# Optimization experiments

Measured on AMD Instinct MI355X. Metric: run time of the kernel, lower is better.

Reference implementation:

```python
import jax, jax.numpy as jnp
import numpy as np


def _hilbert_d2xy(n, d):
    # standard Hilbert curve: distance d -> (x, y) on n x n grid (n power of 2)
    x = y = 0
    t = d
    s = 1
    while s < n:
        rx = 1 & (t // 2)
        ry = 1 & (t ^ rx)
        if ry == 0:
            if rx == 1:
                x = s - 1 - x
                y = s - 1 - y
            x, y = y, x
        x += s * rx
        y += s * ry
        t //= 4
        s *= 2
    return x, y


def _hilbert_perm(seq_len):
    n = int(round(np.sqrt(seq_len)))
    assert n * n == seq_len
    perm = np.empty(seq_len, dtype=np.int32)
    for d in range(seq_len):
        x, y = _hilbert_d2xy(n, d)
        perm[d] = y * n + x  # linear (row-major) index visited at Hilbert step d
    return perm


def setup_inputs() -> dict:
    key = jax.random.key(0)
    k1, k2, k3 = jax.random.split(key, 3)
    B, S, H, D = 1, 4096, 8, 64
    q = jax.random.normal(k1, (B, S, H, D), dtype=jnp.float32)
    k = jax.random.normal(k2, (B, S, H, D), dtype=jnp.float32)
    v = jax.random.normal(k3, (B, S, H, D), dtype=jnp.float32)
    hilbert_perm = jnp.asarray(_hilbert_perm(S))
    return {"q": q, "k": k, "v": v, "hilbert_perm": hilbert_perm}


def reference(q, k, v, hilbert_perm):
    B, S, H, D = q.shape
    inv_perm = jnp.argsort(hilbert_perm)

    # apply_hilbert_ordering along dim=1 (seq): gather by permutation
    q_o = q[:, hilbert_perm]
    k_o = k[:, hilbert_perm]
    v_o = v[:, hilbert_perm]

    # faithful to original: raw flat reshape of [B,S,H,D] -> [B*H, S, D]
    q_f = q_o.reshape(B * H, S, D)
    k_f = k_o.reshape(B * H, S, D)
    v_f = v_o.reshape(B * H, S, D)

    scale = 1.0 / jnp.sqrt(jnp.asarray(D, dtype=q.dtype))
    scores = jnp.einsum('bsd,btd->bst', q_f, k_f) * scale  # [B*H, S, S]
    attn = jax.nn.softmax(scores, axis=-1)
    out_f = jnp.einsum('bst,btd->bsd', attn, v_f)  # [B*H, S, D]

    out = out_f.reshape(B, H, S, D).transpose(0, 2, 1, 3).reshape(B, S, H, D)
    # inverse Hilbert ordering along dim=1
    return out[:, inv_perm]
```

## Files before the change

### kernel.cpp

```cpp
#include <hip/hip_runtime.h>

typedef _Float16 f16;
typedef _Float16 f16x4 __attribute__((ext_vector_type(4)));
typedef _Float16 f16x8 __attribute__((ext_vector_type(8)));
typedef __fp16 fp16x2 __attribute__((ext_vector_type(2)));
typedef float f32x4 __attribute__((ext_vector_type(4)));

#define MFMA_16x16x32_F16(A, B, C) __builtin_amdgcn_mfma_f32_16x16x32_f16((A), (B), (C), 0, 0, 0)

typedef const __attribute__((address_space(1))) char gchar;
typedef __attribute__((address_space(3))) char lchar;

__device__ __forceinline__ float fexp2(float x) { return __builtin_amdgcn_exp2f(x); }
__device__ __forceinline__ int swzb(int b) { return b ^ ((b >> 3) & 0x70); }

namespace {
constexpr int SB = 4096;
constexpr size_t BB = (size_t)SB * 64 * 2;
}

__device__ __forceinline__ int kinv(int r) {
    return 32 * (r >> 5) + 8 * ((r >> 2) & 3) + 4 * ((r >> 4) & 1) + (r & 3);
}

__global__ __launch_bounds__(256)
void hilbert_prepass_kernel(const float* __restrict__ kp, const float* __restrict__ vp,
                            const int* __restrict__ perm,
                            char* __restrict__ kw, char* __restrict__ vtw)
{
    const int bid = blockIdx.x;
    const int batch = bid & 7;
    const int tile = bid >> 3;
    const int tid = (int)threadIdx.x;
    const int r = tid >> 2;
    const int c4 = tid & 3;

    __shared__ float Vl[64][68];

    const int t = tile * 64 + r;
    const int srow = perm[batch * 512 + (t >> 3)];
    const size_t boff = (size_t)srow * 512 + (t & 7) * 64 + c4 * 16;

    {
        const float* ks = kp + boff;
        const float4 k0 = *(const float4*)(ks + 0);
        const float4 k1 = *(const float4*)(ks + 4);
        const float4 k2 = *(const float4*)(ks + 8);
        const float4 k3 = *(const float4*)(ks + 12);
        f16x8 h0, h1;
        h0[0] = (f16)k0.x; h0[1] = (f16)k0.y; h0[2] = (f16)k0.z; h0[3] = (f16)k0.w;
        h0[4] = (f16)k1.x; h0[5] = (f16)k1.y; h0[6] = (f16)k1.z; h0[7] = (f16)k1.w;
        h1[0] = (f16)k2.x; h1[1] = (f16)k2.y; h1[2] = (f16)k2.z; h1[3] = (f16)k2.w;
        h1[4] = (f16)k3.x; h1[5] = (f16)k3.y; h1[6] = (f16)k3.z; h1[7] = (f16)k3.w;
        char* kt = kw + (size_t)batch * BB + (size_t)tile * 8192;
        const int o = r * 128 + c4 * 32;
        *(f16x8*)(kt + swzb(o)) = h0;
        *(f16x8*)(kt + swzb(o + 16)) = h1;
    }
    {
        const float* vs = vp + boff;
        *(float4*)&Vl[r][c4 * 16 + 0]  = *(const float4*)(vs + 0);
        *(float4*)&Vl[r][c4 * 16 + 4]  = *(const float4*)(vs + 4);
        *(float4*)&Vl[r][c4 * 16 + 8]  = *(const float4*)(vs + 8);
        *(float4*)&Vl[r][c4 * 16 + 12] = *(const float4*)(vs + 12);
    }
    __syncthreads();
    {
        const int d = tid >> 2;
        const int a = tid & 3;
        char* vt = vtw + (size_t)batch * BB + (size_t)tile * 8192;
        const int b0 = 32 * (a >> 1) + 4 * (a & 1);
#pragma unroll
        for (int gp = 0; gp < 4; ++gp) {
            f16x4 qv;
#pragma unroll
            for (int v = 0; v < 4; ++v) qv[v] = (f16)Vl[16 * a + 4 * gp + v][d];
            *(f16x4*)(vt + swzb(d * 128 + (b0 + 8 * gp) * 2)) = qv;
        }
    }
}

__global__ __launch_bounds__(1024, 4)
void hilbert_attn_kernel(const float* __restrict__ qp,
                         const int* __restrict__ perm,
                         const char* __restrict__ kw, const char* __restrict__ vtw,
                         float* __restrict__ op)
{
    __shared__ __align__(16) char SM[131072];

    const int bid = blockIdx.x;
    const int batch = bid & 7;
    const int qbase = (bid >> 3) * 128;
    const int tid = (int)threadIdx.x;
    const int w = tid >> 6;
    const int lane = tid & 63;
    const int l16 = lane & 15;
    const int g = lane >> 4;
    const int q = w >> 2;
    const int wq = w & 3;
    const int swz = (l16 & 7) << 4;

    f16x8 Qf0[2], Qf1[2];
    {
        constexpr float qscl = 0.125f * 1.44269504088896340736f;
#pragma unroll
        for (int s = 0; s < 2; ++s) {
            const int t = qbase + wq * 32 + s * 16 + l16;
            const int srow = perm[batch * 512 + (t >> 3)];
            const float* src = qp + (size_t)srow * 512 + (t & 7) * 64 + g * 8;
#pragma unroll
            for (int kt = 0; kt < 2; ++kt) {
                const float4 x0 = *(const float4*)(src + 32 * kt);
                const float4 x1 = *(const float4*)(src + 32 * kt + 4);
                f16x8 f;
                f[0] = (f16)(x0.x * qscl); f[1] = (f16)(x0.y * qscl);
                f[2] = (f16)(x0.z * qscl); f[3] = (f16)(x0.w * qscl);
                f[4] = (f16)(x1.x * qscl); f[5] = (f16)(x1.y * qscl);
                f[6] = (f16)(x1.z * qscl); f[7] = (f16)(x1.w * qscl);
                if (s == 0) Qf0[kt] = f; else Qf1[kt] = f;
            }
        }
    }

    f32x4 oacc0[4], oacc1[4];
#pragma unroll
    for (int i = 0; i < 4; ++i) {
        oacc0[i] = (f32x4){0.f, 0.f, 0.f, 0.f};
        oacc1[i] = (f32x4){0.f, 0.f, 0.f, 0.f};
    }
    float lr0 = 0.f, lr1 = 0.f;

    const char* ksrc = kw + (size_t)batch * BB + (size_t)tid * 16;
    const char* vsrc = vtw + (size_t)batch * BB + (size_t)tid * 16;

    {
        lchar* dst = (lchar*)&SM[w << 10];
#pragma unroll
        for (int c = 0; c < 2; ++c) {
            __builtin_amdgcn_global_load_lds((gchar*)(ksrc + c * 16384), dst + c * 16384, 16, 0, 0);
            __builtin_amdgcn_global_load_lds((gchar*)(vsrc + c * 16384), dst + 32768 + c * 16384, 16, 0, 0);
        }
    }
    __syncthreads();

#pragma unroll 2
    for (int it = 0; it < 16; ++it) {
        const int cur = it & 1;
        const int kbb = cur * 65536 + q * 8192;
        const int vbb = cur * 65536 + 32768 + q * 8192;

        if (it < 15) {
            const size_t go = (size_t)(it + 1) * 32768;
            lchar* dst = (lchar*)&SM[(cur ^ 1) * 65536 + (w << 10)];
#pragma unroll
            for (int c = 0; c < 2; ++c) {
                __builtin_amdgcn_global_load_lds((gchar*)(ksrc + go + c * 16384), dst + c * 16384, 16, 0, 0);
                __builtin_amdgcn_global_load_lds((gchar*)(vsrc + go + c * 16384), dst + 32768 + c * 16384, 16, 0, 0);
            }
        }

        f32x4 sa0[4], sa1[4];
#pragma unroll
        for (int i = 0; i < 4; ++i) {
            sa0[i] = (f32x4){0.f, 0.f, 0.f, 0.f};
            sa1[i] = (f32x4){0.f, 0.f, 0.f, 0.f};
        }
        __builtin_amdgcn_s_setprio(1);
#pragma unroll
        for (int kt = 0; kt < 2; ++kt) {
#pragma unroll
            for (int mt = 0; mt < 4; ++mt) {
                const int off = kbb + (l16 + 16 * mt) * 128 + (((g + 4 * kt) * 16) ^ swz);
                const f16x8 kf = *(const f16x8*)&SM[off];
                sa0[mt] = MFMA_16x16x32_F16(kf, Qf0[kt], sa0[mt]);
                sa1[mt] = MFMA_16x16x32_F16(kf, Qf1[kt], sa1[mt]);
            }
        }
        __builtin_amdgcn_s_setprio(0);

        float e0[16], e1[16];
#pragma unroll
        for (int mt = 0; mt < 4; ++mt) {
#pragma unroll
            for (int v = 0; v < 4; ++v) {
                e0[4 * mt + v] = fexp2(sa0[mt][v]);
                e1[4 * mt + v] = fexp2(sa1[mt][v]);
            }
        }
#pragma unroll
        for (int i = 0; i < 16; ++i) { lr0 += e0[i]; lr1 += e1[i]; }

        union U8 { f16x8 v; fp16x2 h[4]; };
        U8 p0k0, p0k1, p1k0, p1k1;
#pragma unroll
        for (int i = 0; i < 4; ++i) {
            p0k0.h[i] = __builtin_amdgcn_cvt_pkrtz(e0[2 * i], e0[2 * i + 1]);
            p0k1.h[i] = __builtin_amdgcn_cvt_pkrtz(e0[8 + 2 * i], e0[9 + 2 * i]);
            p1k0.h[i] = __builtin_amdgcn_cvt_pkrtz(e1[2 * i], e1[2 * i + 1]);
            p1k1.h[i] = __builtin_amdgcn_cvt_pkrtz(e1[8 + 2 * i], e1[9 + 2 * i]);
        }

        __builtin_amdgcn_s_setprio(1);
#pragma unroll
        for (int kt = 0; kt < 2; ++kt) {
            const f16x8 pf0 = kt ? p0k1.v : p0k0.v;
            const f16x8 pf1 = kt ? p1k1.v : p1k0.v;
#pragma unroll
            for (int mtd = 0; mtd < 4; ++mtd) {
                const int voff = vbb + (l16 + 16 * mtd) * 128 + (((g + 4 * kt) * 16) ^ swz);
                const f16x8 vf = *(const f16x8*)&SM[voff];
                oacc0[mtd] = MFMA_16x16x32_F16(vf, pf0, oacc0[mtd]);
                oacc1[mtd] = MFMA_16x16x32_F16(vf, pf1, oacc1[mtd]);
            }
        }
        __builtin_amdgcn_s_setprio(0);

        __syncthreads();
    }

    lr0 += __shfl_xor(lr0, 16);
    lr0 += __shfl_xor(lr0, 32);
    lr1 += __shfl_xor(lr1, 16);
    lr1 += __shfl_xor(lr1, 32);

    float* OB = (float*)SM;
    float* ML = (float*)&SM[98304];
    if (q >= 1) {
        float* ob = OB + ((q - 1) * 4 + wq) * 2048;
#pragma unroll
        for (int mtd = 0; mtd < 4; ++mtd) {
            *(f32x4*)&ob[l16 * 64 + mtd * 16 + g * 4] = oacc0[mtd];
            *(f32x4*)&ob[(16 + l16) * 64 + mtd * 16 + g * 4] = oacc1[mtd];
        }
        if (g == 0) {
            ML[((q - 1) * 4 + wq) * 32 + l16] = lr0;
            ML[((q - 1) * 4 + wq) * 32 + 16 + l16] = lr1;
        }
    }
    __syncthreads();
    if (q == 0) {
#pragma unroll
        for (int s = 0; s < 2; ++s) {
            float lsum = (s == 0) ? lr0 : lr1;
#pragma unroll
            for (int p = 0; p < 3; ++p) lsum += ML[(p * 4 + wq) * 32 + s * 16 + l16];
            const float linv = 1.f / lsum;
            const int t = qbase + wq * 32 + s * 16 + l16;
            const int srow = perm[t];
            float* dst = op + (size_t)srow * 512 + batch * 64 + 4 * g;
#pragma unroll
            for (int mtd = 0; mtd < 4; ++mtd) {
                f32x4 acc = (s == 0) ? oacc0[mtd] : oacc1[mtd];
#pragma unroll
                for (int p = 0; p < 3; ++p) {
                    const f32x4 o2 = *(const f32x4*)&OB[(p * 4 + wq) * 2048 +
                                                        (s * 16 + l16) * 64 + mtd * 16 + g * 4];
                    acc[0] += o2[0]; acc[1] += o2[1]; acc[2] += o2[2]; acc[3] += o2[3];
                }
                float4 o;
                o.x = acc[0] * linv; o.y = acc[1] * linv;
                o.z = acc[2] * linv; o.w = acc[3] * linv;
                *(float4*)(dst + 16 * mtd) = o;
            }
        }
    }
}

extern "C" void kernel_launch(void* const* d_in, const int* in_sizes, int n_in,
                              void* d_out, int out_size, void* d_ws, size_t ws_size,
                              hipStream_t stream) {
    (void)in_sizes; (void)n_in; (void)out_size; (void)ws_size;
    const float* q = (const float*)d_in[0];
    const float* k = (const float*)d_in[1];
    const float* v = (const float*)d_in[2];
    const int* perm = (const int*)d_in[3];
    float* out = (float*)d_out;
    char* kw = (char*)d_ws;
    char* vtw = kw + 8 * BB;
    hipLaunchKernelGGL(hilbert_prepass_kernel, dim3(512), dim3(256), 0, stream,
                       k, v, perm, kw, vtw);
    hipLaunchKernelGGL(hilbert_attn_kernel, dim3(256), dim3(1024), 0, stream,
                       q, perm, kw, vtw, out);
}
```

Baseline: 52.63 us.

## Split K and V prefetch and use fine-grained vmcnt waits with raw barriers

```diff
diff --git a/kernel.cpp b/kernel.cpp
--- a/kernel.cpp
+++ b/kernel.cpp
@@ -135,28 +135,25 @@
 
     {
         lchar* dst = (lchar*)&SM[w << 10];
-#pragma unroll
-        for (int c = 0; c < 2; ++c) {
-            __builtin_amdgcn_global_load_lds((gchar*)(ksrc + c * 16384), dst + c * 16384, 16, 0, 0);
-            __builtin_amdgcn_global_load_lds((gchar*)(vsrc + c * 16384), dst + 32768 + c * 16384, 16, 0, 0);
-        }
-    }
-    __syncthreads();
+        __builtin_amdgcn_global_load_lds((gchar*)(ksrc), dst, 16, 0, 0);
+        __builtin_amdgcn_global_load_lds((gchar*)(ksrc + 16384), dst + 16384, 16, 0, 0);
+        __builtin_amdgcn_global_load_lds((gchar*)(vsrc), dst + 32768, 16, 0, 0);
+        __builtin_amdgcn_global_load_lds((gchar*)(vsrc + 16384), dst + 49152, 16, 0, 0);
+    }
+    asm volatile("s_waitcnt vmcnt(0)" ::: "memory");
+    __builtin_amdgcn_s_barrier();
 
 #pragma unroll 2
     for (int it = 0; it < 16; ++it) {
         const int cur = it & 1;
         const int kbb = cur * 65536 + q * 8192;
         const int vbb = cur * 65536 + 32768 + q * 8192;
+        const size_t go = (size_t)(it + 1) * 32768;
+        lchar* dstb = (lchar*)&SM[(cur ^ 1) * 65536 + (w << 10)];
 
         if (it < 15) {
-            const size_t go = (size_t)(it + 1) * 32768;
-            lchar* dst = (lchar*)&SM[(cur ^ 1) * 65536 + (w << 10)];
-#pragma unroll
-            for (int c = 0; c < 2; ++c) {
-                __builtin_amdgcn_global_load_lds((gchar*)(ksrc + go + c * 16384), dst + c * 16384, 16, 0, 0);
-                __builtin_amdgcn_global_load_lds((gchar*)(vsrc + go + c * 16384), dst + 32768 + c * 16384, 16, 0, 0);
-            }
+            __builtin_amdgcn_global_load_lds((gchar*)(ksrc + go), dstb, 16, 0, 0);
+            __builtin_amdgcn_global_load_lds((gchar*)(ksrc + go + 16384), dstb + 16384, 16, 0, 0);
         }
 
         f32x4 sa0[4], sa1[4];
@@ -178,6 +175,11 @@
         }
         __builtin_amdgcn_s_setprio(0);
 
+        if (it < 15) {
+            __builtin_amdgcn_global_load_lds((gchar*)(vsrc + go), dstb + 32768, 16, 0, 0);
+            __builtin_amdgcn_global_load_lds((gchar*)(vsrc + go + 16384), dstb + 49152, 16, 0, 0);
+        }
+
         float e0[16], e1[16];
 #pragma unroll
         for (int mt = 0; mt < 4; ++mt) {
@@ -200,6 +202,12 @@
             p1k1.h[i] = __builtin_amdgcn_cvt_pkrtz(e1[8 + 2 * i], e1[9 + 2 * i]);
         }
 
+        if (it > 0) {
+            if (it < 15) { asm volatile("s_waitcnt vmcnt(2)" ::: "memory"); }
+            else         { asm volatile("s_waitcnt vmcnt(0)" ::: "memory"); }
+            __builtin_amdgcn_s_barrier();
+        }
+
         __builtin_amdgcn_s_setprio(1);
 #pragma unroll
         for (int kt = 0; kt < 2; ++kt) {
@@ -215,13 +223,18 @@
         }
         __builtin_amdgcn_s_setprio(0);
 
-        __syncthreads();
+        if (it < 15) {
+            asm volatile("s_waitcnt vmcnt(2)" ::: "memory");
+            __builtin_amdgcn_s_barrier();
+        }
     }
 
     lr0 += __shfl_xor(lr0, 16);
     lr0 += __shfl_xor(lr0, 32);
     lr1 += __shfl_xor(lr1, 16);
     lr1 += __shfl_xor(lr1, 32);
+
+    __syncthreads();
 
     float* OB = (float*)SM;
     float* ML = (float*)&SM[98304];
```

New measurement: 106.1 us. +101.6%, slower.

## Halve attention block to 512 threads with 64 query rows per wave

Applied to the files above, without the earlier changes.

```diff
diff --git a/kernel.cpp b/kernel.cpp
--- a/kernel.cpp
+++ b/kernel.cpp
@@ -80,7 +80,7 @@
     }
 }
 
-__global__ __launch_bounds__(1024, 4)
+__global__ __launch_bounds__(512, 2)
 void hilbert_attn_kernel(const float* __restrict__ qp,
                          const int* __restrict__ perm,
                          const char* __restrict__ kw, const char* __restrict__ vtw,
@@ -96,16 +96,16 @@
     const int lane = tid & 63;
     const int l16 = lane & 15;
     const int g = lane >> 4;
-    const int q = w >> 2;
-    const int wq = w & 3;
+    const int Kq = w >> 1;
+    const int wq = w & 1;
     const int swz = (l16 & 7) << 4;
 
-    f16x8 Qf0[2], Qf1[2];
+    f16x8 Qf[4][2];
     {
         constexpr float qscl = 0.125f * 1.44269504088896340736f;
 #pragma unroll
-        for (int s = 0; s < 2; ++s) {
-            const int t = qbase + wq * 32 + s * 16 + l16;
+        for (int s = 0; s < 4; ++s) {
+            const int t = qbase + wq * 64 + s * 16 + l16;
             const int srow = perm[batch * 512 + (t >> 3)];
             const float* src = qp + (size_t)srow * 512 + (t & 7) * 64 + g * 8;
 #pragma unroll
@@ -117,143 +117,183 @@
                 f[2] = (f16)(x0.z * qscl); f[3] = (f16)(x0.w * qscl);
                 f[4] = (f16)(x1.x * qscl); f[5] = (f16)(x1.y * qscl);
                 f[6] = (f16)(x1.z * qscl); f[7] = (f16)(x1.w * qscl);
-                if (s == 0) Qf0[kt] = f; else Qf1[kt] = f;
-            }
-        }
-    }
-
-    f32x4 oacc0[4], oacc1[4];
-#pragma unroll
-    for (int i = 0; i < 4; ++i) {
-        oacc0[i] = (f32x4){0.f, 0.f, 0.f, 0.f};
-        oacc1[i] = (f32x4){0.f, 0.f, 0.f, 0.f};
-    }
-    float lr0 = 0.f, lr1 = 0.f;
+                Qf[s][kt] = f;
+            }
+        }
+    }
+
+    f32x4 oacc[4][4];
+#pragma unroll
+    for (int s = 0; s < 4; ++s)
+#pragma unroll
+        for (int i = 0; i < 4; ++i) oacc[s][i] = (f32x4){0.f, 0.f, 0.f, 0.f};
+    float lr[4] = {0.f, 0.f, 0.f, 0.f};
 
     const char* ksrc = kw + (size_t)batch * BB + (size_t)tid * 16;
     const char* vsrc = vtw + (size_t)batch * BB + (size_t)tid * 16;
 
+    union U8 { f16x8 v; fp16x2 h[4]; };
+
     {
         lchar* dst = (lchar*)&SM[w << 10];
 #pragma unroll
-        for (int c = 0; c < 2; ++c) {
-            __builtin_amdgcn_global_load_lds((gchar*)(ksrc + c * 16384), dst + c * 16384, 16, 0, 0);
-            __builtin_amdgcn_global_load_lds((gchar*)(vsrc + c * 16384), dst + 32768 + c * 16384, 16, 0, 0);
-        }
-    }
-    __syncthreads();
-
-#pragma unroll 2
-    for (int it = 0; it < 16; ++it) {
+        for (int c = 0; c < 4; ++c) {
+            __builtin_amdgcn_global_load_lds((gchar*)(ksrc + c * 8192), dst + c * 8192, 16, 0, 0);
+            __builtin_amdgcn_global_load_lds((gchar*)(vsrc + c * 8192), dst + 32768 + c * 8192, 16, 0, 0);
+        }
+    }
+    asm volatile("s_waitcnt vmcnt(0)" ::: "memory");
+    __builtin_amdgcn_s_barrier();
+
+    for (int it = 0; it < 15; ++it) {
         const int cur = it & 1;
-        const int kbb = cur * 65536 + q * 8192;
-        const int vbb = cur * 65536 + 32768 + q * 8192;
-
-        if (it < 15) {
-            const size_t go = (size_t)(it + 1) * 32768;
-            lchar* dst = (lchar*)&SM[(cur ^ 1) * 65536 + (w << 10)];
-#pragma unroll
-            for (int c = 0; c < 2; ++c) {
-                __builtin_amdgcn_global_load_lds((gchar*)(ksrc + go + c * 16384), dst + c * 16384, 16, 0, 0);
-                __builtin_amdgcn_global_load_lds((gchar*)(vsrc + go + c * 16384), dst + 32768 + c * 16384, 16, 0, 0);
-            }
-        }
-
-        f32x4 sa0[4], sa1[4];
-#pragma unroll
-        for (int i = 0; i < 4; ++i) {
-            sa0[i] = (f32x4){0.f, 0.f, 0.f, 0.f};
-            sa1[i] = (f32x4){0.f, 0.f, 0.f, 0.f};
-        }
-        __builtin_amdgcn_s_setprio(1);
-#pragma unroll
-        for (int kt = 0; kt < 2; ++kt) {
-#pragma unroll
-            for (int mt = 0; mt < 4; ++mt) {
+        const int kbb = cur * 65536 + Kq * 8192;
+        const int vbb = cur * 65536 + 32768 + Kq * 8192;
+        const size_t go = (size_t)(it + 1) * 32768;
+        lchar* dstb = (lchar*)&SM[(cur ^ 1) * 65536 + (w << 10)];
+
+#pragma unroll
+        for (int c = 0; c < 4; ++c)
+            __builtin_amdgcn_global_load_lds((gchar*)(ksrc + go + c * 8192), dstb + c * 8192, 16, 0, 0);
+
+        U8 Pk0[4], Pk1[4];
+#pragma unroll
+        for (int mt = 0; mt < 4; ++mt) {
+            f32x4 sa[4];
+#pragma unroll
+            for (int s = 0; s < 4; ++s) sa[s] = (f32x4){0.f, 0.f, 0.f, 0.f};
+            __builtin_amdgcn_s_setprio(1);
+#pragma unroll
+            for (int kt = 0; kt < 2; ++kt) {
                 const int off = kbb + (l16 + 16 * mt) * 128 + (((g + 4 * kt) * 16) ^ swz);
                 const f16x8 kf = *(const f16x8*)&SM[off];
-                sa0[mt] = MFMA_16x16x32_F16(kf, Qf0[kt], sa0[mt]);
-                sa1[mt] = MFMA_16x16x32_F16(kf, Qf1[kt], sa1[mt]);
-            }
-        }
-        __builtin_amdgcn_s_setprio(0);
-
-        float e0[16], e1[16];
-#pragma unroll
-        for (int mt = 0; mt < 4; ++mt) {
-#pragma unroll
-            for (int v = 0; v < 4; ++v) {
-                e0[4 * mt + v] = fexp2(sa0[mt][v]);
-                e1[4 * mt + v] = fexp2(sa1[mt][v]);
-            }
-        }
-#pragma unroll
-        for (int i = 0; i < 16; ++i) { lr0 += e0[i]; lr1 += e1[i]; }
-
-        union U8 { f16x8 v; fp16x2 h[4]; };
-        U8 p0k0, p0k1, p1k0, p1k1;
-#pragma unroll
-        for (int i = 0; i < 4; ++i) {
-            p0k0.h[i] = __builtin_amdgcn_cvt_pkrtz(e0[2 * i], e0[2 * i + 1]);
-            p0k1.h[i] = __builtin_amdgcn_cvt_pkrtz(e0[8 + 2 * i], e0[9 + 2 * i]);
-            p1k0.h[i] = __builtin_amdgcn_cvt_pkrtz(e1[2 * i], e1[2 * i + 1]);
-            p1k1.h[i] = __builtin_amdgcn_cvt_pkrtz(e1[8 + 2 * i], e1[9 + 2 * i]);
-        }
+#pragma unroll
+                for (int s = 0; s < 4; ++s) sa[s] = MFMA_16x16x32_F16(kf, Qf[s][kt], sa[s]);
+            }
+            __builtin_amdgcn_s_setprio(0);
+#pragma unroll
+            for (int s = 0; s < 4; ++s) {
+                const float a0 = fexp2(sa[s][0]);
+                const float a1 = fexp2(sa[s][1]);
+                const float a2 = fexp2(sa[s][2]);
+                const float a3 = fexp2(sa[s][3]);
+                lr[s] += (a0 + a1) + (a2 + a3);
+                const fp16x2 h0 = __builtin_amdgcn_cvt_pkrtz(a0, a1);
+                const fp16x2 h1 = __builtin_amdgcn_cvt_pkrtz(a2, a3);
+                if (mt < 2) { Pk0[s].h[2 * mt] = h0; Pk0[s].h[2 * mt + 1] = h1; }
+                else        { Pk1[s].h[2 * (mt - 2)] = h0; Pk1[s].h[2 * (mt - 2) + 1] = h1; }
+            }
+        }
+
+#pragma unroll
+        for (int c = 0; c < 4; ++c)
+            __builtin_amdgcn_global_load_lds((gchar*)(vsrc + go + c * 8192), dstb + 32768 + c * 8192, 16, 0, 0);
+
+        asm volatile("s_waitcnt vmcnt(8)" ::: "memory");
+        __builtin_amdgcn_s_barrier();
 
         __builtin_amdgcn_s_setprio(1);
 #pragma unroll
         for (int kt = 0; kt < 2; ++kt) {
-            const f16x8 pf0 = kt ? p0k1.v : p0k0.v;
-            const f16x8 pf1 = kt ? p1k1.v : p1k0.v;
 #pragma unroll
             for (int mtd = 0; mtd < 4; ++mtd) {
                 const int voff = vbb + (l16 + 16 * mtd) * 128 + (((g + 4 * kt) * 16) ^ swz);
                 const f16x8 vf = *(const f16x8*)&SM[voff];
-                oacc0[mtd] = MFMA_16x16x32_F16(vf, pf0, oacc0[mtd]);
-                oacc1[mtd] = MFMA_16x16x32_F16(vf, pf1, oacc1[mtd]);
+#pragma unroll
+                for (int s = 0; s < 4; ++s)
+                    oacc[s][mtd] = MFMA_16x16x32_F16(vf, kt ? Pk1[s].v : Pk0[s].v, oacc[s][mtd]);
             }
         }
         __builtin_amdgcn_s_setprio(0);
 
-        __syncthreads();
-    }
-
-    lr0 += __shfl_xor(lr0, 16);
-    lr0 += __shfl_xor(lr0, 32);
-    lr1 += __shfl_xor(lr1, 16);
-    lr1 += __shfl_xor(lr1, 32);
+        asm volatile("s_waitcnt vmcnt(4)" ::: "memory");
+        __builtin_amdgcn_s_barrier();
+    }
+
+    {
+        const int kbb = 65536 + Kq * 8192;
+        const int vbb = 65536 + 32768 + Kq * 8192;
+
+        U8 Pk0[4], Pk1[4];
+#pragma unroll
+        for (int mt = 0; mt < 4; ++mt) {
+            f32x4 sa[4];
+#pragma unroll
+            for (int s = 0; s < 4; ++s) sa[s] = (f32x4){0.f, 0.f, 0.f, 0.f};
+#pragma unroll
+            for (int kt = 0; kt < 2; ++kt) {
+                const int off = kbb + (l16 + 16 * mt) * 128 + (((g + 4 * kt) * 16) ^ swz);
+                const f16x8 kf = *(const f16x8*)&SM[off];
+#pragma unroll
+                for (int s = 0; s < 4; ++s) sa[s] = MFMA_16x16x32_F16(kf, Qf[s][kt], sa[s]);
+            }
+#pragma unroll
+            for (int s = 0; s < 4; ++s) {
+                const float a0 = fexp2(sa[s][0]);
+                const float a1 = fexp2(sa[s][1]);
+                const float a2 = fexp2(sa[s][2]);
+                const float a3 = fexp2(sa[s][3]);
+                lr[s] += (a0 + a1) + (a2 + a3);
+                const fp16x2 h0 = __builtin_amdgcn_cvt_pkrtz(a0, a1);
+                const fp16x2 h1 = __builtin_amdgcn_cvt_pkrtz(a2, a3);
+                if (mt < 2) { Pk0[s].h[2 * mt] = h0; Pk0[s].h[2 * mt + 1] = h1; }
+                else        { Pk1[s].h[2 * (mt - 2)] = h0; Pk1[s].h[2 * (mt - 2) + 1] = h1; }
+            }
+        }
+        asm volatile("s_waitcnt vmcnt(0)" ::: "memory");
+        __builtin_amdgcn_s_barrier();
+#pragma unroll
+        for (int kt = 0; kt < 2; ++kt) {
+#pragma unroll
+            for (int mtd = 0; mtd < 4; ++mtd) {
+                const int voff = vbb + (l16 + 16 * mtd) * 128 + (((g + 4 * kt) * 16) ^ swz);
+                const f16x8 vf = *(const f16x8*)&SM[voff];
+#pragma unroll
+                for (int s = 0; s < 4; ++s)
+                    oacc[s][mtd] = MFMA_16x16x32_F16(vf, kt ? Pk1[s].v : Pk0[s].v, oacc[s][mtd]);
+            }
+        }
+    }
+
+#pragma unroll
+    for (int s = 0; s < 4; ++s) {
+        lr[s] += __shfl_xor(lr[s], 16);
+        lr[s] += __shfl_xor(lr[s], 32);
+    }
+
+    __syncthreads();
 
     float* OB = (float*)SM;
     float* ML = (float*)&SM[98304];
-    if (q >= 1) {
-        float* ob = OB + ((q - 1) * 4 + wq) * 2048;
-#pragma unroll
-        for (int mtd = 0; mtd < 4; ++mtd) {
-            *(f32x4*)&ob[l16 * 64 + mtd * 16 + g * 4] = oacc0[mtd];
-            *(f32x4*)&ob[(16 + l16) * 64 + mtd * 16 + g * 4] = oacc1[mtd];
-        }
-        if (g == 0) {
-            ML[((q - 1) * 4 + wq) * 32 + l16] = lr0;
-            ML[((q - 1) * 4 + wq) * 32 + 16 + l16] = lr1;
-        }
+    if (Kq >= 1) {
+        float* ob = OB + ((Kq - 1) * 2 + wq) * 4096;
+#pragma unroll
+        for (int s = 0; s < 4; ++s)
+#pragma unroll
+            for (int mtd = 0; mtd < 4; ++mtd)
+                *(f32x4*)&ob[(s * 16 + l16) * 64 + mtd * 16 + g * 4] = oacc[s][mtd];
+        if (g == 0)
+#pragma unroll
+            for (int s = 0; s < 4; ++s)
+                ML[((Kq - 1) * 2 + wq) * 64 + s * 16 + l16] = lr[s];
     }
     __syncthreads();
-    if (q == 0) {
-#pragma unroll
-        for (int s = 0; s < 2; ++s) {
-            float lsum = (s == 0) ? lr0 : lr1;
-#pragma unroll
-            for (int p = 0; p < 3; ++p) lsum += ML[(p * 4 + wq) * 32 + s * 16 + l16];
+    if (Kq == 0) {
+#pragma unroll
+        for (int s = 0; s < 4; ++s) {
+            float lsum = lr[s];
+#pragma unroll
+            for (int p = 0; p < 3; ++p) lsum += ML[(p * 2 + wq) * 64 + s * 16 + l16];
             const float linv = 1.f / lsum;
-            const int t = qbase + wq * 32 + s * 16 + l16;
+            const int t = qbase + wq * 64 + s * 16 + l16;
             const int srow = perm[t];
             float* dst = op + (size_t)srow * 512 + batch * 64 + 4 * g;
 #pragma unroll
             for (int mtd = 0; mtd < 4; ++mtd) {
-                f32x4 acc = (s == 0) ? oacc0[mtd] : oacc1[mtd];
+                f32x4 acc = oacc[s][mtd];
 #pragma unroll
                 for (int p = 0; p < 3; ++p) {
-                    const f32x4 o2 = *(const f32x4*)&OB[(p * 4 + wq) * 2048 +
+                    const f32x4 o2 = *(const f32x4*)&OB[(p * 2 + wq) * 4096 +
                                                         (s * 16 + l16) * 64 + mtd * 16 + g * 4];
                     acc[0] += o2[0]; acc[1] += o2[1]; acc[2] += o2[2]; acc[3] += o2[3];
                 }
@@ -279,6 +319,6 @@
     char* vtw = kw + 8 * BB;
     hipLaunchKernelGGL(hilbert_prepass_kernel, dim3(512), dim3(256), 0, stream,
                        k, v, perm, kw, vtw);
-    hipLaunchKernelGGL(hilbert_attn_kernel, dim3(256), dim3(1024), 0, stream,
+    hipLaunchKernelGGL(hilbert_attn_kernel, dim3(256), dim3(512), 0, stream,
                        q, perm, kw, vtw, out);
 }
```

After: 51.55 us. 2.1% less time.
